# Kernel optimization log

Hardware: AMD Instinct MI355X
Metric: run time of the kernel (lower is better)

Reference implementation:

```python
import jax, jax.numpy as jnp
import numpy as np

B, T, E, H = 8, 2048, 1024, 128

def setup_inputs() -> dict:
    key = jax.random.key(0)
    kx, kq, kk, kv = jax.random.split(key, 4)
    x = jax.random.normal(kx, (B, T, E), dtype=jnp.float32)
    # Linear(E, H, bias=False) weights, stored as (E, H) so y = x @ W
    s = 1.0 / np.sqrt(E)
    Wq = jax.random.normal(kq, (E, H), dtype=jnp.float32) * s
    Wk = jax.random.normal(kk, (E, H), dtype=jnp.float32) * s
    Wv = jax.random.normal(kv, (E, H), dtype=jnp.float32) * s
    return {"x": x, "Wq": Wq, "Wk": Wk, "Wv": Wv}

def reference(x, Wq, Wk, Wv):
    # x: (B, T, E)
    Tcur = x.shape[1]
    q = jnp.einsum('bte,eh->bth', x, Wq)
    k = jnp.einsum('bte,eh->bth', x, Wk)
    v = jnp.einsum('bte,eh->bth', x, Wv)
    scores = jnp.einsum('bqh,bkh->bqk', q, k)  # (B, T, T)
    # NOTE: source multiplies by x.shape[2]**0.5 where x.shape[2] == T here
    scores = scores * jnp.sqrt(jnp.asarray(Tcur, dtype=scores.dtype))
    causal = jnp.tril(jnp.ones((Tcur, Tcur), dtype=bool))
    scores = jnp.where(causal, scores, -jnp.inf)
    attn = jax.nn.softmax(scores, axis=2)
    # dropout p=0.0 -> identity
    return jnp.einsum('bqk,bkh->bqh', attn, v)
```

## Files before the change

### kernel.cpp

```cpp
#include <hip/hip_runtime.h>
#include <hip/hip_bf16.h>
#include <math.h>

#define B_ 8
#define T_ 2048
#define E_ 1024
#define H_ 128
#define M_ (B_*T_)
#define SCALE_ 45.25483399593904f
#define SEG_ 4

typedef __attribute__((ext_vector_type(8))) short bf16x8;
typedef __attribute__((ext_vector_type(4))) float f32x4;

#define mfma16(A, Bv, C) __builtin_amdgcn_mfma_f32_16x16x32_bf16((A), (Bv), (C), 0, 0, 0)

__device__ __forceinline__ ushort bf16_rne(float f) {
  unsigned u = __float_as_uint(f);
  u += 0x7fffu + ((u >> 16) & 1u);
  return (ushort)(u >> 16);
}
__device__ __forceinline__ float bf16_tof(ushort h) {
  return __uint_as_float(((unsigned)h) << 16);
}

template <int N>
__device__ __forceinline__ float ror16(float x) {
  return __uint_as_float((unsigned)__builtin_amdgcn_update_dpp(
      0, (int)__float_as_uint(x), 0x120 + N, 0xF, 0xF, true));
}
__device__ __forceinline__ float rowmax16(float x) {
  x = fmaxf(x, ror16<8>(x));
  x = fmaxf(x, ror16<4>(x));
  x = fmaxf(x, ror16<2>(x));
  x = fmaxf(x, ror16<1>(x));
  return x;
}
__device__ __forceinline__ float rowsum16(float x) {
  x += ror16<8>(x);
  x += ror16<4>(x);
  x += ror16<2>(x);
  x += ror16<1>(x);
  return x;
}

__global__ __launch_bounds__(256) void wsplit(
    const float* __restrict__ Wq, const float* __restrict__ Wk,
    const float* __restrict__ Wv,
    ushort* __restrict__ whT, ushort* __restrict__ wlT)
{
  const int idx = blockIdx.x * 256 + threadIdx.x;
  const int mat = idx / 16384;
  const int rem = idx % 16384;
  const int n   = rem >> 7;
  const int k0  = (rem & 127) * 8;
  const float* W = (mat == 0) ? Wq : (mat == 1) ? Wk : Wv;
  bf16x8 hv, lv;
  #pragma unroll
  for (int j = 0; j < 8; ++j) {
    const float f = W[(size_t)(k0 + j) * H_ + n];
    const ushort h = bf16_rne(f);
    hv[j] = (short)h;
    lv[j] = (short)bf16_rne(f - bf16_tof(h));
  }
  const size_t off = ((size_t)mat * H_ + n) * E_ + k0;
  *(bf16x8*)(whT + off) = hv;
  *(bf16x8*)(wlT + off) = lv;
}

__global__ __launch_bounds__(256) void proj_fused(
    const float* __restrict__ x,
    const ushort* __restrict__ whT, const ushort* __restrict__ wlT,
    ushort* __restrict__ qh, ushort* __restrict__ ql,
    ushort* __restrict__ kh, ushort* __restrict__ kl,
    ushort* __restrict__ vT)
{
  const int m0   = blockIdx.x * 64;
  const int half = blockIdx.y;
  const int tid  = threadIdx.x;
  const int wave = tid >> 6, lane = tid & 63;
  const int quad = lane >> 4, l15 = lane & 15;

  __shared__ __align__(16) ushort SM[20480];
  ushort* AhS = SM;
  ushort* AlS = SM + 2560;
  ushort* BhS = SM + 5120;
  ushort* BlS = SM + 12800;

  const int nlc = (half == 0) ? 768 : 256;

  f32x4 acc[3][4];
  #pragma unroll
  for (int j = 0; j < 3; ++j)
    #pragma unroll
    for (int mt = 0; mt < 4; ++mt) acc[j][mt] = (f32x4){0.f, 0.f, 0.f, 0.f};

  const int arow  = tid >> 2;
  const int akoff = (tid & 3) * 8;

  float4 f0, f1;
  bf16x8 bh[3], bl[3];
  {
    const float* srcx = x + (size_t)(m0 + arow) * E_ + akoff;
    f0 = *(const float4*)srcx;
    f1 = *(const float4*)(srcx + 4);
    #pragma unroll
    for (int u = 0; u < 3; ++u) {
      const int c = u * 256 + tid;
      bh[u] = *(const bf16x8*)(whT + (size_t)(half*192 + (c >> 2)) * E_ + (c & 3) * 8);
      if (c < nlc)
        bl[u] = *(const bf16x8*)(wlT + (size_t)(half*192 + (c >> 2)) * E_ + (c & 3) * 8);
    }
  }

  for (int k0 = 0; k0 < E_; k0 += 32) {
    __syncthreads();

    {
      const float f[8] = {f0.x, f0.y, f0.z, f0.w, f1.x, f1.y, f1.z, f1.w};
      bf16x8 hv, lv;
      #pragma unroll
      for (int j = 0; j < 8; ++j) {
        const ushort h = bf16_rne(f[j]);
        hv[j] = (short)h;
        lv[j] = (short)bf16_rne(f[j] - bf16_tof(h));
      }
      *(bf16x8*)&AhS[arow * 40 + akoff] = hv;
      *(bf16x8*)&AlS[arow * 40 + akoff] = lv;
    }
    #pragma unroll
    for (int u = 0; u < 3; ++u) {
      const int c = u * 256 + tid;
      *(bf16x8*)&BhS[(c >> 2) * 40 + (c & 3) * 8] = bh[u];
      if (c < nlc)
        *(bf16x8*)&BlS[(c >> 2) * 40 + (c & 3) * 8] = bl[u];
    }
    __syncthreads();

    if (k0 + 32 < E_) {
      const int kn = k0 + 32;
      const float* srcx = x + (size_t)(m0 + arow) * E_ + kn + akoff;
      f0 = *(const float4*)srcx;
      f1 = *(const float4*)(srcx + 4);
      #pragma unroll
      for (int u = 0; u < 3; ++u) {
        const int c = u * 256 + tid;
        bh[u] = *(const bf16x8*)(whT + (size_t)(half*192 + (c >> 2)) * E_ + kn + (c & 3) * 8);
        if (c < nlc)
          bl[u] = *(const bf16x8*)(wlT + (size_t)(half*192 + (c >> 2)) * E_ + kn + (c & 3) * 8);
      }
    }

    bf16x8 a_h[4], a_l[4];
    #pragma unroll
    for (int mt = 0; mt < 4; ++mt) {
      a_h[mt] = *(const bf16x8*)&AhS[(mt * 16 + l15) * 40 + quad * 8];
      a_l[mt] = *(const bf16x8*)&AlS[(mt * 16 + l15) * 40 + quad * 8];
    }
    #pragma unroll
    for (int j = 0; j < 3; ++j) {
      const int ntl = wave + 4 * j;
      const int g   = half * 12 + ntl;
      const bf16x8 b_h = *(const bf16x8*)&BhS[(ntl * 16 + l15) * 40 + quad * 8];
      if (g < 16) {
        const bf16x8 b_l = *(const bf16x8*)&BlS[(ntl * 16 + l15) * 40 + quad * 8];
        #pragma unroll
        for (int mt = 0; mt < 4; ++mt) {
          acc[j][mt] = mfma16(a_h[mt], b_h, acc[j][mt]);
          acc[j][mt] = mfma16(a_h[mt], b_l, acc[j][mt]);
          acc[j][mt] = mfma16(a_l[mt], b_h, acc[j][mt]);
        }
      } else {
        #pragma unroll
        for (int mt = 0; mt < 4; ++mt)
          acc[j][mt] = mfma16(a_h[mt], b_h, acc[j][mt]);
      }
    }
  }

  #pragma unroll
  for (int j = 0; j < 3; ++j) {
    const int g = half * 12 + wave + 4 * j;
    if (g < 16) {
      ushort* oh = (g < 8) ? qh : kh;
      ushort* ol = (g < 8) ? ql : kl;
      const int ncol = (g & 7) * 16 + l15;
      #pragma unroll
      for (int mt = 0; mt < 4; ++mt)
        #pragma unroll
        for (int r = 0; r < 4; ++r) {
          const float a = acc[j][mt][r];
          const ushort h = bf16_rne(a);
          const size_t off = (size_t)(m0 + mt * 16 + quad * 4 + r) * H_ + ncol;
          oh[off] = h;
          ol[off] = bf16_rne(a - bf16_tof(h));
        }
    }
  }
  if (half == 1) {
    __syncthreads();
    ushort* smT = SM;
    #pragma unroll
    for (int j = 1; j < 3; ++j) {
      const int g = 12 + wave + 4 * j;
      const int hcol = (g - 16) * 16 + l15;
      #pragma unroll
      for (int mt = 0; mt < 4; ++mt)
        #pragma unroll
        for (int r = 0; r < 4; ++r)
          smT[hcol * 64 + mt * 16 + quad * 4 + r] = bf16_rne(acc[j][mt][r]);
    }
    __syncthreads();
    const int b  = m0 >> 11;
    const int t0 = m0 & 2047;
    #pragma unroll
    for (int u = 0; u < 4; ++u) {
      const int c    = u * 256 + tid;
      const int n    = c >> 3;
      const int toff = (c & 7) * 8;
      *(bf16x8*)(vT + ((size_t)b * H_ + n) * T_ + t0 + toff) =
          *(const bf16x8*)&smT[n * 64 + toff];
    }
  }
}

__global__ __launch_bounds__(256) void attn_flash(
    const ushort* __restrict__ qh, const ushort* __restrict__ ql,
    const ushort* __restrict__ kh, const ushort* __restrict__ kl,
    const ushort* __restrict__ vT,
    ushort* __restrict__ Opart, float* __restrict__ mlpart)
{
  const int b    = (int)blockIdx.x & 7;
  const int seg  = (int)blockIdx.x >> 3;
  const int qt   = 31 - (int)blockIdx.y;
  const int q0   = qt * 64;
  const int tid  = threadIdx.x;
  const int wave = tid >> 6, lane = tid & 63;
  const int quad = lane >> 4, l15 = lane & 15;
  const f32x4 z4 = (f32x4){0.f, 0.f, 0.f, 0.f};

  __shared__ __align__(16) ushort KhS[32 * 132];
  __shared__ __align__(16) ushort KlS[32 * 132];
  __shared__ __align__(16) ushort VtS[128 * 40];
  __shared__ __align__(16) ushort smP[4 * 640];

  const int ntiles = 2 * qt + 2;
  const int cnt    = (ntiles + SEG_ - 1) >> 2;
  const int jt0    = seg * cnt;
  const int jt1    = (jt0 + cnt < ntiles) ? (jt0 + cnt) : ntiles;

  const int q0w  = q0 + wave * 16;
  const int ntw  = ((q0w + 15) >> 5) + 1;
  const size_t pidx = ((size_t)(b * 128 + qt * 4 + wave)) * SEG_ + seg;
  ushort* op = Opart + pidx * 2048;
  float*  ml = mlpart + pidx * 32;

  if (jt0 >= jt1) {
    const bf16x8 zz = {0, 0, 0, 0, 0, 0, 0, 0};
    #pragma unroll
    for (int u = 0; u < 4; ++u)
      *(bf16x8*)(op + lane * 32 + u * 8) = zz;
    if (lane < 32) ml[lane] = (lane & 1) ? 0.f : -1e30f;
    return;
  }

  const size_t base = (size_t)b * T_ * H_;

  const ushort* qhp = qh + base + (size_t)(q0w + l15) * H_ + quad * 8;
  const ushort* qlp = ql + base + (size_t)(q0w + l15) * H_ + quad * 8;
  bf16x8 Qh[4], Ql[4];
  #pragma unroll
  for (int c = 0; c < 4; ++c) {
    Qh[c] = *(const bf16x8*)(qhp + c * 32);
    Ql[c] = *(const bf16x8*)(qlp + c * 32);
  }

  f32x4 O[8];
  #pragma unroll
  for (int i = 0; i < 8; ++i) O[i] = z4;
  float mstate[4] = {-1e30f, -1e30f, -1e30f, -1e30f};
  float lstate[4] = {0.f, 0.f, 0.f, 0.f};

  bf16x8 rkh[2], rkl[2], rv[2];
  {
    const int k0 = jt0 * 32;
    #pragma unroll
    for (int u = 0; u < 2; ++u) {
      const int c = u * 256 + tid;
      rkh[u] = *(const bf16x8*)(kh + base + (size_t)(k0 + (c >> 4)) * H_ + (c & 15) * 8);
      rkl[u] = *(const bf16x8*)(kl + base + (size_t)(k0 + (c >> 4)) * H_ + (c & 15) * 8);
      rv[u]  = *(const bf16x8*)(vT + base + (size_t)(c >> 2) * T_ + k0 + (c & 3) * 8);
    }
  }

  for (int jt = jt0; jt < jt1; ++jt) {
    __syncthreads();
    #pragma unroll
    for (int u = 0; u < 2; ++u) {
      const int c = u * 256 + tid;
      *(bf16x8*)&KhS[(c >> 4) * 132 + (c & 15) * 8] = rkh[u];
      *(bf16x8*)&KlS[(c >> 4) * 132 + (c & 15) * 8] = rkl[u];
      *(bf16x8*)&VtS[(c >> 2) * 40  + (c & 3) * 8]  = rv[u];
    }
    __syncthreads();

    if (jt + 1 < jt1) {
      const int kn = (jt + 1) * 32;
      #pragma unroll
      for (int u = 0; u < 2; ++u) {
        const int c = u * 256 + tid;
        rkh[u] = *(const bf16x8*)(kh + base + (size_t)(kn + (c >> 4)) * H_ + (c & 15) * 8);
        rkl[u] = *(const bf16x8*)(kl + base + (size_t)(kn + (c >> 4)) * H_ + (c & 15) * 8);
        rv[u]  = *(const bf16x8*)(vT + base + (size_t)(c >> 2) * T_ + kn + (c & 3) * 8);
      }
    }

    if (jt < ntw) {
      const int k0 = jt * 32;
      f32x4 shh0 = z4, shh1 = z4, sx0 = z4, sx1 = z4;
      #pragma unroll
      for (int c = 0; c < 4; ++c) {
        const bf16x8 kh0 = *(const bf16x8*)&KhS[l15 * 132 + c * 32 + quad * 8];
        const bf16x8 kh1 = *(const bf16x8*)&KhS[(16 + l15) * 132 + c * 32 + quad * 8];
        const bf16x8 kl0 = *(const bf16x8*)&KlS[l15 * 132 + c * 32 + quad * 8];
        const bf16x8 kl1 = *(const bf16x8*)&KlS[(16 + l15) * 132 + c * 32 + quad * 8];
        shh0 = mfma16(Qh[c], kh0, shh0);
        shh1 = mfma16(Qh[c], kh1, shh1);
        sx0  = mfma16(Qh[c], kl0, sx0);
        sx1  = mfma16(Qh[c], kl1, sx1);
        sx0  = mfma16(Ql[c], kh0, sx0);
        sx1  = mfma16(Ql[c], kh1, sx1);
      }

      float s0[4], s1[4];
      #pragma unroll
      for (int r = 0; r < 4; ++r) {
        s0[r] = (shh0[r] + sx0[r]) * SCALE_;
        s1[r] = (shh1[r] + sx1[r]) * SCALE_;
      }
      if (jt == ntw - 1) {
        const int krel0 = k0 + l15      - q0w - quad * 4;
        const int krel1 = k0 + 16 + l15 - q0w - quad * 4;
        #pragma unroll
        for (int r = 0; r < 4; ++r) {
          if (krel0 > r) s0[r] = -1e30f;
          if (krel1 > r) s1[r] = -1e30f;
        }
      }

      float alpha[4];
      #pragma unroll
      for (int r = 0; r < 4; ++r) {
        const float rm   = rowmax16(fmaxf(s0[r], s1[r]));
        const float mnew = fmaxf(mstate[r], rm);
        alpha[r] = __expf(mstate[r] - mnew);
        mstate[r] = mnew;
        const float p0 = __expf(s0[r] - mnew);
        const float p1 = __expf(s1[r] - mnew);
        lstate[r] = lstate[r] * alpha[r] + rowsum16(p0 + p1);
        smP[wave * 640 + (quad * 4 + r) * 40 + l15]      = bf16_rne(p0);
        smP[wave * 640 + (quad * 4 + r) * 40 + 16 + l15] = bf16_rne(p1);
      }
      #pragma unroll
      for (int ct = 0; ct < 8; ++ct) {
        O[ct][0] *= alpha[0]; O[ct][1] *= alpha[1];
        O[ct][2] *= alpha[2]; O[ct][3] *= alpha[3];
      }
      const bf16x8 pA = *(const bf16x8*)&smP[wave * 640 + l15 * 40 + quad * 8];
      #pragma unroll
      for (int ct = 0; ct < 8; ++ct) {
        const bf16x8 vf = *(const bf16x8*)&VtS[(ct * 16 + l15) * 40 + quad * 8];
        O[ct] = mfma16(pA, vf, O[ct]);
      }
    }
  }

  #pragma unroll
  for (int r = 0; r < 4; ++r)
    #pragma unroll
    for (int ct = 0; ct < 8; ++ct)
      op[(quad * 4 + r) * 128 + ct * 16 + l15] = bf16_rne(O[ct][r]);
  if (l15 == 0) {
    #pragma unroll
    for (int r = 0; r < 4; ++r) {
      ml[(quad * 4 + r) * 2]     = mstate[r];
      ml[(quad * 4 + r) * 2 + 1] = lstate[r];
    }
  }
}

__global__ __launch_bounds__(256) void attn_combine(
    const ushort* __restrict__ Opart, const float* __restrict__ mlpart,
    float* __restrict__ out)
{
  const int idx = blockIdx.x * 256 + threadIdx.x;
  const int c4  = idx & 31;
  const int r   = idx >> 5;
  const int t   = r & 2047;
  const int qt  = t >> 4, r16 = t & 15;
  const size_t pb = ((size_t)((r >> 11) * 128 + qt)) * SEG_;

  float m[SEG_], l[SEG_];
  #pragma unroll
  for (int s = 0; s < SEG_; ++s) {
    m[s] = mlpart[(pb + s) * 32 + r16 * 2];
    l[s] = mlpart[(pb + s) * 32 + r16 * 2 + 1];
  }
  float M = m[0];
  #pragma unroll
  for (int s = 1; s < SEG_; ++s) M = fmaxf(M, m[s]);
  float w[SEG_], L = 0.f;
  #pragma unroll
  for (int s = 0; s < SEG_; ++s) {
    w[s] = __expf(m[s] - M);
    L += l[s] * w[s];
  }
  float4 acc = make_float4(0.f, 0.f, 0.f, 0.f);
  #pragma unroll
  for (int s = 0; s < SEG_; ++s) {
    const ushort4 o = *(const ushort4*)(Opart + (pb + s) * 2048 + r16 * 128 + c4 * 4);
    acc.x += w[s] * bf16_tof(o.x);
    acc.y += w[s] * bf16_tof(o.y);
    acc.z += w[s] * bf16_tof(o.z);
    acc.w += w[s] * bf16_tof(o.w);
  }
  const float inv = 1.0f / L;
  *(float4*)(out + (size_t)r * H_ + c4 * 4) =
      make_float4(acc.x * inv, acc.y * inv, acc.z * inv, acc.w * inv);
}

extern "C" void kernel_launch(void* const* d_in, const int* in_sizes, int n_in,
                              void* d_out, int out_size, void* d_ws, size_t ws_size,
                              hipStream_t stream) {
  (void)in_sizes; (void)n_in; (void)out_size; (void)ws_size;
  const float* x  = (const float*)d_in[0];
  const float* Wq = (const float*)d_in[1];
  const float* Wk = (const float*)d_in[2];
  const float* Wv = (const float*)d_in[3];
  float* out = (float*)d_out;

  ushort* qhb = (ushort*)d_ws;
  ushort* qlb = qhb + (size_t)M_ * H_;
  ushort* khb = qlb + (size_t)M_ * H_;
  ushort* klb = khb + (size_t)M_ * H_;
  ushort* vTb = klb + (size_t)M_ * H_;
  ushort* whT = vTb + (size_t)M_ * H_;
  ushort* wlT = whT + (size_t)3 * H_ * E_;
  ushort* Opart = wlT + (size_t)3 * H_ * E_;
  float*  mlpart = (float*)(Opart + (size_t)B_ * 128 * SEG_ * 2048);

  wsplit<<<dim3(192), 256, 0, stream>>>(Wq, Wk, Wv, whT, wlT);
  proj_fused<<<dim3(M_/64, 2), 256, 0, stream>>>(x, whT, wlT,
                                                 qhb, qlb, khb, klb, vTb);
  attn_flash<<<dim3(B_*SEG_, 32), 256, 0, stream>>>(qhb, qlb, khb, klb, vTb,
                                                    Opart, mlpart);
  attn_combine<<<dim3(2048), 256, 0, stream>>>(Opart, mlpart, out);
}
```

Before: 186.2 us.

## Store weights, K and V in MFMA fragment order to bypass LDS staging

Weights are pre-split into a layout where each lane's MFMA B-fragment is one contiguous 16-byte chunk. The projection kernel therefore loads B operands straight from global memory into registers, double-buffered through the macro, and no longer stages them in shared memory. K and V are written in fragment order too, so the attention kernel does linear shared-memory stores and conflict-free per-lane fragment reads without padded strides. The gain is less LDS traffic and bank conflicts in both kernels. The cost is scattered 2-byte global stores for K in the projection epilogue and more registers held per thread.

```diff
diff --git a/kernel.cpp b/kernel.cpp
--- a/kernel.cpp
+++ b/kernel.cpp
@@ -15,6 +15,10 @@
 
 #define mfma16(A, Bv, C) __builtin_amdgcn_mfma_f32_16x16x32_bf16((A), (Bv), (C), 0, 0, 0)
 
+#define FRAGW(g, kc, lane)  ((((size_t)(g)*32 + (kc))*64 + (lane))*8)
+#define FRAGK(b, kt16, kc, lane) (((((size_t)(b)*128 + (kt16))*4 + (kc))*64 + (lane))*8)
+#define FRAGV(b, ht, kt32, lane) (((((size_t)(b)*8 + (ht))*64 + (kt32))*64 + (lane))*8)
+
 __device__ __forceinline__ ushort bf16_rne(float f) {
   unsigned u = __float_as_uint(f);
   u += 0x7fffu + ((u >> 16) & 1u);
@@ -49,12 +53,16 @@
     const float* __restrict__ Wv,
     ushort* __restrict__ whT, ushort* __restrict__ wlT)
 {
-  const int idx = blockIdx.x * 256 + threadIdx.x;
-  const int mat = idx / 16384;
-  const int rem = idx % 16384;
-  const int n   = rem >> 7;
-  const int k0  = (rem & 127) * 8;
+  const int idx  = blockIdx.x * 256 + threadIdx.x;
+  const int mat  = idx >> 14;
+  const int rem  = idx & 16383;
+  const int nt   = rem >> 11;
+  const int kc   = (rem >> 6) & 31;
+  const int lane = rem & 63;
+  const int quad = lane >> 4, l15 = lane & 15;
   const float* W = (mat == 0) ? Wq : (mat == 1) ? Wk : Wv;
+  const int n  = nt * 16 + l15;
+  const int k0 = kc * 32 + quad * 8;
   bf16x8 hv, lv;
   #pragma unroll
   for (int j = 0; j < 8; ++j) {
@@ -63,17 +71,68 @@
     hv[j] = (short)h;
     lv[j] = (short)bf16_rne(f - bf16_tof(h));
   }
-  const size_t off = ((size_t)mat * H_ + n) * E_ + k0;
-  *(bf16x8*)(whT + off) = hv;
-  *(bf16x8*)(wlT + off) = lv;
-}
+  *(bf16x8*)(whT + (size_t)idx * 8) = hv;
+  *(bf16x8*)(wlT + (size_t)idx * 8) = lv;
+}
+
+#define PSTEP(KC, BH, BL, BHN, BLN) do {                                      \
+    __syncthreads();                                                          \
+    {                                                                         \
+      const float f_[8] = {xf0.x, xf0.y, xf0.z, xf0.w,                        \
+                           xf1.x, xf1.y, xf1.z, xf1.w};                       \
+      bf16x8 hv_, lv_;                                                        \
+      _Pragma("unroll")                                                       \
+      for (int jj_ = 0; jj_ < 8; ++jj_) {                                     \
+        const ushort h_ = bf16_rne(f_[jj_]);                                  \
+        hv_[jj_] = (short)h_;                                                 \
+        lv_[jj_] = (short)bf16_rne(f_[jj_] - bf16_tof(h_));                   \
+      }                                                                       \
+      *(bf16x8*)&AhS[ca * 8] = hv_;                                           \
+      *(bf16x8*)&AlS[ca * 8] = lv_;                                           \
+    }                                                                         \
+    __syncthreads();                                                          \
+    if ((KC) + 1 < 32) {                                                      \
+      const float* s_ = x + (size_t)(m0 + arow) * E_ + ((KC) + 1) * 32 + akoff;\
+      xf0 = *(const float4*)s_;                                               \
+      xf1 = *(const float4*)(s_ + 4);                                         \
+      _Pragma("unroll")                                                       \
+      for (int j_ = 0; j_ < 3; ++j_) {                                        \
+        const int g_ = g0 + 4 * j_;                                           \
+        BHN[j_] = *(const bf16x8*)(whT + FRAGW(g_, (KC) + 1, lane));          \
+        if (g_ < 16)                                                          \
+          BLN[j_] = *(const bf16x8*)(wlT + FRAGW(g_, (KC) + 1, lane));        \
+      }                                                                       \
+    }                                                                         \
+    bf16x8 a_h_[4], a_l_[4];                                                  \
+    _Pragma("unroll")                                                         \
+    for (int mt_ = 0; mt_ < 4; ++mt_) {                                       \
+      a_h_[mt_] = *(const bf16x8*)&AhS[(((mt_ * 4 + quad) * 16) + l15) * 8];  \
+      a_l_[mt_] = *(const bf16x8*)&AlS[(((mt_ * 4 + quad) * 16) + l15) * 8];  \
+    }                                                                         \
+    _Pragma("unroll")                                                         \
+    for (int j_ = 0; j_ < 3; ++j_) {                                          \
+      const int g_ = g0 + 4 * j_;                                             \
+      if (g_ < 16) {                                                          \
+        _Pragma("unroll")                                                     \
+        for (int mt_ = 0; mt_ < 4; ++mt_) {                                   \
+          acc[j_][mt_] = mfma16(a_h_[mt_], BH[j_], acc[j_][mt_]);             \
+          acc[j_][mt_] = mfma16(a_h_[mt_], BL[j_], acc[j_][mt_]);             \
+          acc[j_][mt_] = mfma16(a_l_[mt_], BH[j_], acc[j_][mt_]);             \
+        }                                                                     \
+      } else {                                                                \
+        _Pragma("unroll")                                                     \
+        for (int mt_ = 0; mt_ < 4; ++mt_)                                     \
+          acc[j_][mt_] = mfma16(a_h_[mt_], BH[j_], acc[j_][mt_]);             \
+      }                                                                       \
+    }                                                                         \
+  } while (0)
 
 __global__ __launch_bounds__(256) void proj_fused(
     const float* __restrict__ x,
     const ushort* __restrict__ whT, const ushort* __restrict__ wlT,
     ushort* __restrict__ qh, ushort* __restrict__ ql,
-    ushort* __restrict__ kh, ushort* __restrict__ kl,
-    ushort* __restrict__ vT)
+    ushort* __restrict__ kfh, ushort* __restrict__ kfl,
+    ushort* __restrict__ vF)
 {
   const int m0   = blockIdx.x * 64;
   const int half = blockIdx.y;
@@ -81,13 +140,9 @@
   const int wave = tid >> 6, lane = tid & 63;
   const int quad = lane >> 4, l15 = lane & 15;
 
-  __shared__ __align__(16) ushort SM[20480];
+  __shared__ __align__(16) ushort SM[9216];
   ushort* AhS = SM;
-  ushort* AlS = SM + 2560;
-  ushort* BhS = SM + 5120;
-  ushort* BlS = SM + 12800;
-
-  const int nlc = (half == 0) ? 768 : 256;
+  ushort* AlS = SM + 2048;
 
   f32x4 acc[3][4];
   #pragma unroll
@@ -97,94 +152,34 @@
 
   const int arow  = tid >> 2;
   const int akoff = (tid & 3) * 8;
-
-  float4 f0, f1;
-  bf16x8 bh[3], bl[3];
+  const int ca    = ((arow >> 4) * 4 + (tid & 3)) * 16 + (arow & 15);
+  const int g0    = half * 12 + wave;
+
+  float4 xf0, xf1;
+  bf16x8 bhA[3], blA[3], bhB[3], blB[3];
   {
-    const float* srcx = x + (size_t)(m0 + arow) * E_ + akoff;
-    f0 = *(const float4*)srcx;
-    f1 = *(const float4*)(srcx + 4);
-    #pragma unroll
-    for (int u = 0; u < 3; ++u) {
-      const int c = u * 256 + tid;
-      bh[u] = *(const bf16x8*)(whT + (size_t)(half*192 + (c >> 2)) * E_ + (c & 3) * 8);
-      if (c < nlc)
-        bl[u] = *(const bf16x8*)(wlT + (size_t)(half*192 + (c >> 2)) * E_ + (c & 3) * 8);
-    }
-  }
-
-  for (int k0 = 0; k0 < E_; k0 += 32) {
-    __syncthreads();
-
-    {
-      const float f[8] = {f0.x, f0.y, f0.z, f0.w, f1.x, f1.y, f1.z, f1.w};
-      bf16x8 hv, lv;
-      #pragma unroll
-      for (int j = 0; j < 8; ++j) {
-        const ushort h = bf16_rne(f[j]);
-        hv[j] = (short)h;
-        lv[j] = (short)bf16_rne(f[j] - bf16_tof(h));
-      }
-      *(bf16x8*)&AhS[arow * 40 + akoff] = hv;
-      *(bf16x8*)&AlS[arow * 40 + akoff] = lv;
-    }
-    #pragma unroll
-    for (int u = 0; u < 3; ++u) {
-      const int c = u * 256 + tid;
-      *(bf16x8*)&BhS[(c >> 2) * 40 + (c & 3) * 8] = bh[u];
-      if (c < nlc)
-        *(bf16x8*)&BlS[(c >> 2) * 40 + (c & 3) * 8] = bl[u];
-    }
-    __syncthreads();
-
-    if (k0 + 32 < E_) {
-      const int kn = k0 + 32;
-      const float* srcx = x + (size_t)(m0 + arow) * E_ + kn + akoff;
-      f0 = *(const float4*)srcx;
-      f1 = *(const float4*)(srcx + 4);
-      #pragma unroll
-      for (int u = 0; u < 3; ++u) {
-        const int c = u * 256 + tid;
-        bh[u] = *(const bf16x8*)(whT + (size_t)(half*192 + (c >> 2)) * E_ + kn + (c & 3) * 8);
-        if (c < nlc)
-          bl[u] = *(const bf16x8*)(wlT + (size_t)(half*192 + (c >> 2)) * E_ + kn + (c & 3) * 8);
-      }
-    }
-
-    bf16x8 a_h[4], a_l[4];
-    #pragma unroll
-    for (int mt = 0; mt < 4; ++mt) {
-      a_h[mt] = *(const bf16x8*)&AhS[(mt * 16 + l15) * 40 + quad * 8];
-      a_l[mt] = *(const bf16x8*)&AlS[(mt * 16 + l15) * 40 + quad * 8];
-    }
+    const float* s = x + (size_t)(m0 + arow) * E_ + akoff;
+    xf0 = *(const float4*)s;
+    xf1 = *(const float4*)(s + 4);
     #pragma unroll
     for (int j = 0; j < 3; ++j) {
-      const int ntl = wave + 4 * j;
-      const int g   = half * 12 + ntl;
-      const bf16x8 b_h = *(const bf16x8*)&BhS[(ntl * 16 + l15) * 40 + quad * 8];
-      if (g < 16) {
-        const bf16x8 b_l = *(const bf16x8*)&BlS[(ntl * 16 + l15) * 40 + quad * 8];
-        #pragma unroll
-        for (int mt = 0; mt < 4; ++mt) {
-          acc[j][mt] = mfma16(a_h[mt], b_h, acc[j][mt]);
-          acc[j][mt] = mfma16(a_h[mt], b_l, acc[j][mt]);
-          acc[j][mt] = mfma16(a_l[mt], b_h, acc[j][mt]);
-        }
-      } else {
-        #pragma unroll
-        for (int mt = 0; mt < 4; ++mt)
-          acc[j][mt] = mfma16(a_h[mt], b_h, acc[j][mt]);
-      }
-    }
+      const int g = g0 + 4 * j;
+      bhA[j] = *(const bf16x8*)(whT + FRAGW(g, 0, lane));
+      if (g < 16) blA[j] = *(const bf16x8*)(wlT + FRAGW(g, 0, lane));
+    }
+  }
+
+  int kc = 0;
+  while (true) {
+    PSTEP(kc, bhA, blA, bhB, blB); if (++kc == 32) break;
+    PSTEP(kc, bhB, blB, bhA, blA); if (++kc == 32) break;
   }
 
   #pragma unroll
   for (int j = 0; j < 3; ++j) {
-    const int g = half * 12 + wave + 4 * j;
-    if (g < 16) {
-      ushort* oh = (g < 8) ? qh : kh;
-      ushort* ol = (g < 8) ? ql : kl;
-      const int ncol = (g & 7) * 16 + l15;
+    const int g = g0 + 4 * j;
+    if (g < 8) {
+      const int ncol = g * 16 + l15;
       #pragma unroll
       for (int mt = 0; mt < 4; ++mt)
         #pragma unroll
@@ -192,8 +187,25 @@
           const float a = acc[j][mt][r];
           const ushort h = bf16_rne(a);
           const size_t off = (size_t)(m0 + mt * 16 + quad * 4 + r) * H_ + ncol;
-          oh[off] = h;
-          ol[off] = bf16_rne(a - bf16_tof(h));
+          qh[off] = h;
+          ql[off] = bf16_rne(a - bf16_tof(h));
+        }
+    } else if (g < 16) {
+      const int hcol = (g - 8) * 16 + l15;
+      const int kch  = hcol >> 5;
+      const int qdh  = (hcol >> 3) & 3;
+      const int jj   = hcol & 7;
+      #pragma unroll
+      for (int mt = 0; mt < 4; ++mt)
+        #pragma unroll
+        for (int r = 0; r < 4; ++r) {
+          const float a = acc[j][mt][r];
+          const int tg = m0 + mt * 16 + quad * 4 + r;
+          const int bb = tg >> 11, tl = tg & 2047;
+          const size_t ad = FRAGK(bb, tl >> 4, kch, qdh * 16 + (tl & 15)) + jj;
+          const ushort h = bf16_rne(a);
+          kfh[ad] = h;
+          kfl[ad] = bf16_rne(a - bf16_tof(h));
         }
     }
   }
@@ -208,26 +220,27 @@
       for (int mt = 0; mt < 4; ++mt)
         #pragma unroll
         for (int r = 0; r < 4; ++r)
-          smT[hcol * 64 + mt * 16 + quad * 4 + r] = bf16_rne(acc[j][mt][r]);
+          smT[hcol * 72 + mt * 16 + quad * 4 + r] = bf16_rne(acc[j][mt][r]);
     }
     __syncthreads();
-    const int b  = m0 >> 11;
-    const int t0 = m0 & 2047;
+    const int bb = m0 >> 11, t0 = m0 & 2047;
     #pragma unroll
     for (int u = 0; u < 4; ++u) {
-      const int c    = u * 256 + tid;
-      const int n    = c >> 3;
-      const int toff = (c & 7) * 8;
-      *(bf16x8*)(vT + ((size_t)b * H_ + n) * T_ + t0 + toff) =
-          *(const bf16x8*)&smT[n * 64 + toff];
+      const int c   = u * 256 + tid;
+      const int ht  = c >> 7;
+      const int ktl = (c >> 6) & 1;
+      const int lv  = c & 63;
+      const int qv  = lv >> 4, l15v = lv & 15;
+      *(bf16x8*)(vF + FRAGV(bb, ht, (t0 >> 5) + ktl, lv)) =
+          *(const bf16x8*)&smT[(ht * 16 + l15v) * 72 + ktl * 32 + qv * 8];
     }
   }
 }
 
 __global__ __launch_bounds__(256) void attn_flash(
     const ushort* __restrict__ qh, const ushort* __restrict__ ql,
-    const ushort* __restrict__ kh, const ushort* __restrict__ kl,
-    const ushort* __restrict__ vT,
+    const ushort* __restrict__ kfh, const ushort* __restrict__ kfl,
+    const ushort* __restrict__ vF,
     ushort* __restrict__ Opart, float* __restrict__ mlpart)
 {
   const int b    = (int)blockIdx.x & 7;
@@ -239,9 +252,9 @@
   const int quad = lane >> 4, l15 = lane & 15;
   const f32x4 z4 = (f32x4){0.f, 0.f, 0.f, 0.f};
 
-  __shared__ __align__(16) ushort KhS[32 * 132];
-  __shared__ __align__(16) ushort KlS[32 * 132];
-  __shared__ __align__(16) ushort VtS[128 * 40];
+  __shared__ __align__(16) ushort KhS[4096];
+  __shared__ __align__(16) ushort KlS[4096];
+  __shared__ __align__(16) ushort VtS[4096];
   __shared__ __align__(16) ushort smP[4 * 640];
 
   const int ntiles = 2 * qt + 2;
@@ -249,8 +262,8 @@
   const int jt0    = seg * cnt;
   const int jt1    = (jt0 + cnt < ntiles) ? (jt0 + cnt) : ntiles;
 
-  const int q0w  = q0 + wave * 16;
-  const int ntw  = ((q0w + 15) >> 5) + 1;
+  const int q0w = q0 + wave * 16;
+  const int ntw = ((q0w + 15) >> 5) + 1;
   const size_t pidx = ((size_t)(b * 128 + qt * 4 + wave)) * SEG_ + seg;
   ushort* op = Opart + pidx * 2048;
   float*  ml = mlpart + pidx * 32;
@@ -283,13 +296,12 @@
 
   bf16x8 rkh[2], rkl[2], rv[2];
   {
-    const int k0 = jt0 * 32;
     #pragma unroll
     for (int u = 0; u < 2; ++u) {
       const int c = u * 256 + tid;
-      rkh[u] = *(const bf16x8*)(kh + base + (size_t)(k0 + (c >> 4)) * H_ + (c & 15) * 8);
-      rkl[u] = *(const bf16x8*)(kl + base + (size_t)(k0 + (c >> 4)) * H_ + (c & 15) * 8);
-      rv[u]  = *(const bf16x8*)(vT + base + (size_t)(c >> 2) * T_ + k0 + (c & 3) * 8);
+      rkh[u] = *(const bf16x8*)(kfh + FRAGK(b, 2 * jt0 + (c >> 8), (c >> 6) & 3, c & 63));
+      rkl[u] = *(const bf16x8*)(kfl + FRAGK(b, 2 * jt0 + (c >> 8), (c >> 6) & 3, c & 63));
+      rv[u]  = *(const bf16x8*)(vF  + FRAGV(b, c >> 6, jt0, c & 63));
     }
   }
 
@@ -298,20 +310,19 @@
     #pragma unroll
     for (int u = 0; u < 2; ++u) {
       const int c = u * 256 + tid;
-      *(bf16x8*)&KhS[(c >> 4) * 132 + (c & 15) * 8] = rkh[u];
-      *(bf16x8*)&KlS[(c >> 4) * 132 + (c & 15) * 8] = rkl[u];
-      *(bf16x8*)&VtS[(c >> 2) * 40  + (c & 3) * 8]  = rv[u];
+      *(bf16x8*)&KhS[c * 8] = rkh[u];
+      *(bf16x8*)&KlS[c * 8] = rkl[u];
+      *(bf16x8*)&VtS[c * 8] = rv[u];
     }
     __syncthreads();
 
     if (jt + 1 < jt1) {
-      const int kn = (jt + 1) * 32;
       #pragma unroll
       for (int u = 0; u < 2; ++u) {
         const int c = u * 256 + tid;
-        rkh[u] = *(const bf16x8*)(kh + base + (size_t)(kn + (c >> 4)) * H_ + (c & 15) * 8);
-        rkl[u] = *(const bf16x8*)(kl + base + (size_t)(kn + (c >> 4)) * H_ + (c & 15) * 8);
-        rv[u]  = *(const bf16x8*)(vT + base + (size_t)(c >> 2) * T_ + kn + (c & 3) * 8);
+        rkh[u] = *(const bf16x8*)(kfh + FRAGK(b, 2 * (jt + 1) + (c >> 8), (c >> 6) & 3, c & 63));
+        rkl[u] = *(const bf16x8*)(kfl + FRAGK(b, 2 * (jt + 1) + (c >> 8), (c >> 6) & 3, c & 63));
+        rv[u]  = *(const bf16x8*)(vF  + FRAGV(b, c >> 6, jt + 1, c & 63));
       }
     }
 
@@ -320,10 +331,10 @@
       f32x4 shh0 = z4, shh1 = z4, sx0 = z4, sx1 = z4;
       #pragma unroll
       for (int c = 0; c < 4; ++c) {
-        const bf16x8 kh0 = *(const bf16x8*)&KhS[l15 * 132 + c * 32 + quad * 8];
-        const bf16x8 kh1 = *(const bf16x8*)&KhS[(16 + l15) * 132 + c * 32 + quad * 8];
-        const bf16x8 kl0 = *(const bf16x8*)&KlS[l15 * 132 + c * 32 + quad * 8];
-        const bf16x8 kl1 = *(const bf16x8*)&KlS[(16 + l15) * 132 + c * 32 + quad * 8];
+        const bf16x8 kh0 = *(const bf16x8*)&KhS[(c * 64 + lane) * 8];
+        const bf16x8 kh1 = *(const bf16x8*)&KhS[((4 + c) * 64 + lane) * 8];
+        const bf16x8 kl0 = *(const bf16x8*)&KlS[(c * 64 + lane) * 8];
+        const bf16x8 kl1 = *(const bf16x8*)&KlS[((4 + c) * 64 + lane) * 8];
         shh0 = mfma16(Qh[c], kh0, shh0);
         shh1 = mfma16(Qh[c], kh1, shh1);
         sx0  = mfma16(Qh[c], kl0, sx0);
@@ -369,7 +380,7 @@
       const bf16x8 pA = *(const bf16x8*)&smP[wave * 640 + l15 * 40 + quad * 8];
       #pragma unroll
       for (int ct = 0; ct < 8; ++ct) {
-        const bf16x8 vf = *(const bf16x8*)&VtS[(ct * 16 + l15) * 40 + quad * 8];
+        const bf16x8 vf = *(const bf16x8*)&VtS[(ct * 64 + lane) * 8];
         O[ct] = mfma16(pA, vf, O[ct]);
       }
     }
@@ -441,18 +452,18 @@
 
   ushort* qhb = (ushort*)d_ws;
   ushort* qlb = qhb + (size_t)M_ * H_;
-  ushort* khb = qlb + (size_t)M_ * H_;
-  ushort* klb = khb + (size_t)M_ * H_;
-  ushort* vTb = klb + (size_t)M_ * H_;
-  ushort* whT = vTb + (size_t)M_ * H_;
+  ushort* kfh = qlb + (size_t)M_ * H_;
+  ushort* kfl = kfh + (size_t)M_ * H_;
+  ushort* vFb = kfl + (size_t)M_ * H_;
+  ushort* whT = vFb + (size_t)M_ * H_;
   ushort* wlT = whT + (size_t)3 * H_ * E_;
   ushort* Opart = wlT + (size_t)3 * H_ * E_;
   float*  mlpart = (float*)(Opart + (size_t)B_ * 128 * SEG_ * 2048);
 
   wsplit<<<dim3(192), 256, 0, stream>>>(Wq, Wk, Wv, whT, wlT);
   proj_fused<<<dim3(M_/64, 2), 256, 0, stream>>>(x, whT, wlT,
-                                                 qhb, qlb, khb, klb, vTb);
-  attn_flash<<<dim3(B_*SEG_, 32), 256, 0, stream>>>(qhb, qlb, khb, klb, vTb,
+                                                 qhb, qlb, kfh, kfl, vFb);
+  attn_flash<<<dim3(B_*SEG_, 32), 256, 0, stream>>>(qhb, qlb, kfh, kfl, vFb,
                                                     Opart, mlpart);
   attn_combine<<<dim3(2048), 256, 0, stream>>>(Opart, mlpart, out);
 }
```

After: 184.9 us. No clear change (-0.7%).
